# Kernel optimization log

Hardware: AMD Instinct MI355X
Metric: run time of the kernel (lower is better)

Reference implementation:

```python
import jax, jax.numpy as jnp
import numpy as np

EPS = 1e-12  # matches torch F.normalize eps

def _l2norm(v, axis):
    n = jnp.sqrt(jnp.sum(v * v, axis=axis, keepdims=True))
    return v / jnp.maximum(n, EPS)

def setup_inputs() -> dict:
    key = jax.random.key(0)
    k1, k2, k3 = jax.random.split(key, 3)
    N, D, H, W, K = 64, 128, 60, 80, 64
    x = jax.random.normal(k1, (N, D, H, W), dtype=jnp.float32)
    conv_w = jax.random.normal(k2, (K, D), dtype=jnp.float32) * 0.1
    centroids = jax.random.uniform(k3, (K, D), dtype=jnp.float32)
    return {"x": x, "conv_w": conv_w, "centroids": centroids}

def reference(x, conv_w, centroids):
    N, D, H, W = x.shape
    K = conv_w.shape[0]
    # descriptor-wise L2 normalization over channel dim
    x = _l2norm(x, axis=1)
    xf = x.reshape(N, D, H * W)                       # [N, D, P]
    # 1x1 conv (no bias) == matmul over channels, then softmax over clusters
    logits = jnp.einsum('kd,ndp->nkp', conv_w, xf)    # [N, K, P]
    sa = jax.nn.softmax(logits, axis=1)               # [N, K, P]
    # vlad[n,k,:] = sum_p sa[n,k,p] * (xf[n,:,p] - centroids[k])
    agg = jnp.einsum('nkp,ndp->nkd', sa, xf)          # [N, K, D]
    vlad = agg - sa.sum(axis=-1)[..., None] * centroids[None]
    vlad = _l2norm(vlad, axis=2)                      # intra-normalization
    vlad = vlad.reshape(N, K * D)
    vlad = _l2norm(vlad, axis=1)                      # global L2 norm
    return vlad
```

## Files before the change

kernel.cpp:

```cpp
#include <hip/hip_runtime.h>
#include <hip/hip_bf16.h>
#include <math.h>

#define NN 64
#define DD 128
#define PP 4800
#define KK 64
#define BPN 15
#define PB  320
#define CP  64
#define NCH 5

#define WT  136
#define XPT 136
#define XDT 72
#define SAT 72

#define PAGG_SZ  ((size_t)NN * BPN * KK * DD)
#define PSSUM_SZ ((size_t)NN * BPN * KK)
#define VTMP_SZ  ((size_t)NN * KK * DD)
#define GSUM_SZ  ((size_t)NN * 8)

typedef __attribute__((ext_vector_type(8))) short bf16x8;
typedef __attribute__((ext_vector_type(4))) float f32x4;

__device__ __forceinline__ unsigned short f2bf(float f) {
  unsigned u = __float_as_uint(f);
  u += 0x7fffu + ((u >> 16) & 1u);
  return (unsigned short)(u >> 16);
}
__device__ __forceinline__ unsigned pk2(float a, float b) {
  union { __hip_bfloat162 h2; unsigned u; } cv;
  cv.h2 = __float22bfloat162_rn(make_float2(a, b));
  return cv.u;
}

__global__ __launch_bounds__(256, 2) void main_kernel(const float* __restrict__ x,
                                                      const float* __restrict__ conv_w,
                                                      float* __restrict__ pagg,
                                                      float* __restrict__ pssum) {
  __shared__ __align__(16) unsigned short w_s[KK * WT];
  __shared__ __align__(16) unsigned short xpd[CP * XPT];
  __shared__ __align__(16) unsigned short xdp[DD * XDT];
  __shared__ __align__(16) unsigned short sa_s[KK * SAT];
  __shared__ float red_s[256];

  const int b = blockIdx.x;
  const int n = b / BPN, sl = b % BPN;
  const int t = threadIdx.x, lane = t & 63, wv = t >> 6;
  const int lq = lane >> 4, ll = lane & 15;
  const int pb = t & 7, db = t >> 3;

  {
    int k = t >> 2, h = t & 3;
    const float* wp = conv_w + k * DD + h * 32;
    unsigned short* dst = &w_s[k * WT + h * 32];
#pragma unroll
    for (int i = 0; i < 4; ++i) {
      float4 a = *(const float4*)(wp + 8 * i);
      float4 c = *(const float4*)(wp + 8 * i + 4);
      uint4 o = {pk2(a.x, a.y), pk2(a.z, a.w), pk2(c.x, c.y), pk2(c.z, c.w)};
      *(uint4*)&dst[8 * i] = o;
    }
  }
  if (t < 64) red_s[t] = 0.f;

  const float* xb = x + (size_t)n * DD * PP + (size_t)(4 * db) * PP + sl * PB + 8 * pb;

  float4 pf[8];
#pragma unroll
  for (int r = 0; r < 4; ++r) {
    pf[2 * r]     = *(const float4*)(xb + (size_t)r * PP);
    pf[2 * r + 1] = *(const float4*)(xb + (size_t)r * PP + 4);
  }

  f32x4 acc[8];
#pragma unroll
  for (int i = 0; i < 8; ++i) acc[i] = (f32x4){0.f, 0.f, 0.f, 0.f};
  float ssacc[16];
#pragma unroll
  for (int i = 0; i < 16; ++i) ssacc[i] = 0.f;

  for (int c = 0; c < NCH; ++c) {
    float4 cur[8];
#pragma unroll
    for (int i = 0; i < 8; ++i) cur[i] = pf[i];
    if (c + 1 < NCH) {
      const float* xc = xb + (c + 1) * CP;
#pragma unroll
      for (int r = 0; r < 4; ++r) {
        pf[2 * r]     = *(const float4*)(xc + (size_t)r * PP);
        pf[2 * r + 1] = *(const float4*)(xc + (size_t)r * PP + 4);
      }
    }

    float sq[8];
#pragma unroll
    for (int h = 0; h < 2; ++h)
#pragma unroll
      for (int j = 0; j < 4; ++j) {
        float s = 0.f;
#pragma unroll
        for (int r = 0; r < 4; ++r) {
          float v = (&cur[2 * r + h].x)[j];
          s = fmaf(v, v, s);
        }
        sq[4 * h + j] = s;
      }
#pragma unroll
    for (int i = 0; i < 8; ++i) {
      sq[i] += __shfl_xor(sq[i], 8);
      sq[i] += __shfl_xor(sq[i], 16);
      sq[i] += __shfl_xor(sq[i], 32);
    }

    __syncthreads();

    if (lane < 8) {
#pragma unroll
      for (int j = 0; j < 8; ++j) atomicAdd(&red_s[8 * lane + j], sq[j]);
    }

    {
      unsigned prow[4][4];
#pragma unroll
      for (int r = 0; r < 4; ++r) {
        const float4& a = cur[2 * r];
        const float4& c2 = cur[2 * r + 1];
        prow[r][0] = pk2(a.x, a.y);
        prow[r][1] = pk2(a.z, a.w);
        prow[r][2] = pk2(c2.x, c2.y);
        prow[r][3] = pk2(c2.z, c2.w);
        uint4 o = {prow[r][0], prow[r][1], prow[r][2], prow[r][3]};
        *(uint4*)&xdp[(4 * db + r) * XDT + 8 * pb] = o;
      }
      const int colh = (((db >> 1) ^ pb) << 3) + (db & 1) * 4;
#pragma unroll
      for (int j2 = 0; j2 < 4; ++j2) {
        unsigned lo01 = __builtin_amdgcn_perm(prow[1][j2], prow[0][j2], 0x05040100u);
        unsigned hi01 = __builtin_amdgcn_perm(prow[1][j2], prow[0][j2], 0x07060302u);
        unsigned lo23 = __builtin_amdgcn_perm(prow[3][j2], prow[2][j2], 0x05040100u);
        unsigned hi23 = __builtin_amdgcn_perm(prow[3][j2], prow[2][j2], 0x07060302u);
        int p_e = 8 * pb + 2 * j2;
        *(uint2*)&xpd[p_e * XPT + colh]       = make_uint2(lo01, lo23);
        *(uint2*)&xpd[(p_e + 1) * XPT + colh] = make_uint2(hi01, hi23);
      }
    }
    __syncthreads();

    {
      const int prow_ = wv * 16 + ll;
      const int swz = (2 * wv + (ll >> 3)) & 7;
      f32x4 lg[4];
#pragma unroll
      for (int kt = 0; kt < 4; ++kt) lg[kt] = (f32x4){0.f, 0.f, 0.f, 0.f};
#pragma unroll
      for (int ks = 0; ks < 4; ++ks) {
        bf16x8 bfrag = *(const bf16x8*)&xpd[prow_ * XPT + ((((ks << 2) | lq) ^ swz) << 3)];
#pragma unroll
        for (int kt = 0; kt < 4; ++kt) {
          bf16x8 afrag = *(const bf16x8*)&w_s[(kt * 16 + ll) * WT + ks * 32 + lq * 8];
          lg[kt] = __builtin_amdgcn_mfma_f32_16x16x32_bf16(afrag, bfrag, lg[kt], 0, 0, 0);
        }
      }
      float iv = 1.0f / fmaxf(sqrtf(red_s[prow_]), 1e-12f);
      float vals[16];
      float m = -1e30f;
#pragma unroll
      for (int kt = 0; kt < 4; ++kt)
#pragma unroll
        for (int r = 0; r < 4; ++r) {
          float v = lg[kt][r] * iv;
          vals[kt * 4 + r] = v;
          m = fmaxf(m, v);
        }
      m = fmaxf(m, __shfl_xor(m, 16));
      m = fmaxf(m, __shfl_xor(m, 32));
      float se = 0.f;
#pragma unroll
      for (int i = 0; i < 16; ++i) {
        float e = __expf(vals[i] - m);
        vals[i] = e;
        se += e;
      }
      se += __shfl_xor(se, 16);
      se += __shfl_xor(se, 32);
      float rinv = 1.0f / se;
      float r2 = rinv * iv;
#pragma unroll
      for (int kt = 0; kt < 4; ++kt)
#pragma unroll
        for (int r = 0; r < 4; ++r) {
          float e = vals[kt * 4 + r];
          ssacc[kt * 4 + r] += e * rinv;
          sa_s[(kt * 16 + lq * 4 + r) * SAT + prow_] = f2bf(e * r2);
        }
    }
    __syncthreads();
    if (c + 1 < NCH && t < 64) red_s[t] = 0.f;

#pragma unroll
    for (int ks = 0; ks < 2; ++ks) {
      bf16x8 afrag = *(const bf16x8*)&sa_s[(wv * 16 + ll) * SAT + ks * 32 + lq * 8];
#pragma unroll
      for (int dt = 0; dt < 8; ++dt) {
        bf16x8 bfrag = *(const bf16x8*)&xdp[(dt * 16 + ll) * XDT + ks * 32 + lq * 8];
        acc[dt] = __builtin_amdgcn_mfma_f32_16x16x32_bf16(afrag, bfrag, acc[dt], 0, 0, 0);
      }
    }
  }

  {
    float* base = pagg + (size_t)(n * BPN + sl) * (KK * DD);
#pragma unroll
    for (int dt = 0; dt < 8; ++dt)
#pragma unroll
      for (int r = 0; r < 4; ++r)
        base[(16 * wv + 4 * lq + r) * DD + dt * 16 + ll] = acc[dt][r];
  }
#pragma unroll
  for (int i = 0; i < 16; ++i) {
    float s = ssacc[i];
    s += __shfl_xor(s, 1);
    s += __shfl_xor(s, 2);
    s += __shfl_xor(s, 4);
    s += __shfl_xor(s, 8);
    if (ll == 0) red_s[wv * 64 + (i >> 2) * 16 + lq * 4 + (i & 3)] = s;
  }
  __syncthreads();
  if (t < 64)
    pssum[(n * BPN + sl) * KK + t] =
        red_s[t] + red_s[64 + t] + red_s[128 + t] + red_s[192 + t];
}

__global__ __launch_bounds__(256) void ep1_kernel(const float* __restrict__ pagg,
                                                  const float* __restrict__ pssum,
                                                  const float* __restrict__ cent,
                                                  float* __restrict__ vtmp,
                                                  float* __restrict__ gsum) {
  __shared__ float wsum[4];
  const int blk = blockIdx.x;
  const int n = blk >> 3, kg = blk & 7;
  const int t = threadIdx.x;
  const int kl = t >> 5, c32 = t & 31;
  const int k = kg * 8 + kl;
  const size_t off = (size_t)k * DD + c32 * 4;

  const float* base = pagg + (size_t)n * BPN * (KK * DD) + off;
  float4 a = {0.f, 0.f, 0.f, 0.f};
  for (int s = 0; s < BPN; ++s) {
    float4 v = *(const float4*)(base + (size_t)s * (KK * DD));
    a.x += v.x; a.y += v.y; a.z += v.z; a.w += v.w;
  }
  float sk = 0.f;
  for (int s = 0; s < BPN; ++s) sk += pssum[(n * BPN + s) * KK + k];

  float4 c4 = *(const float4*)(cent + off);
  float4 v;
  v.x = fmaf(-sk, c4.x, a.x);
  v.y = fmaf(-sk, c4.y, a.y);
  v.z = fmaf(-sk, c4.z, a.z);
  v.w = fmaf(-sk, c4.w, a.w);

  float pss = v.x * v.x + v.y * v.y + v.z * v.z + v.w * v.w;
  float ss = pss;
  ss += __shfl_xor(ss, 1);
  ss += __shfl_xor(ss, 2);
  ss += __shfl_xor(ss, 4);
  ss += __shfl_xor(ss, 8);
  ss += __shfl_xor(ss, 16);
  float rinv = 1.0f / fmaxf(sqrtf(ss), 1e-12f);
  v.x *= rinv; v.y *= rinv; v.z *= rinv; v.w *= rinv;
  *(float4*)(vtmp + (size_t)n * (KK * DD) + off) = v;

  float gp = pss * rinv * rinv;
#pragma unroll
  for (int o = 1; o < 64; o <<= 1) gp += __shfl_xor(gp, o);
  if ((t & 63) == 0) wsum[t >> 6] = gp;
  __syncthreads();
  if (t == 0) gsum[blk] = wsum[0] + wsum[1] + wsum[2] + wsum[3];
}

__global__ __launch_bounds__(256) void ep2_kernel(const float* __restrict__ vtmp,
                                                  const float* __restrict__ gsum,
                                                  float* __restrict__ out) {
  const int n = blockIdx.x, t = threadIdx.x;
  const float* gs = gsum + n * 8;
  float g = gs[0] + gs[1] + gs[2] + gs[3] + gs[4] + gs[5] + gs[6] + gs[7];
  float ginv = 1.0f / fmaxf(sqrtf(g), 1e-12f);
  const float4* vi = (const float4*)(vtmp + (size_t)n * (KK * DD));
  float4* vo = (float4*)(out + (size_t)n * (KK * DD));
#pragma unroll
  for (int it = 0; it < 8; ++it) {
    int idx = t + 256 * it;
    float4 f = vi[idx];
    f.x *= ginv; f.y *= ginv; f.z *= ginv; f.w *= ginv;
    vo[idx] = f;
  }
}

extern "C" void kernel_launch(void* const* d_in, const int* in_sizes, int n_in,
                              void* d_out, int out_size, void* d_ws, size_t ws_size,
                              hipStream_t stream) {
  const float* x      = (const float*)d_in[0];
  const float* conv_w = (const float*)d_in[1];
  const float* cent   = (const float*)d_in[2];
  float* out = (float*)d_out;
  float* ws  = (float*)d_ws;

  float* pagg  = ws;
  float* pssum = pagg + PAGG_SZ;
  float* vtmp  = pssum + PSSUM_SZ;
  float* gsum  = vtmp + VTMP_SZ;

  main_kernel<<<NN * BPN, 256, 0, stream>>>(x, conv_w, pagg, pssum);
  ep1_kernel<<<NN * 8, 256, 0, stream>>>(pagg, pssum, cent, vtmp, gsum);
  ep2_kernel<<<NN, 256, 0, stream>>>(vtmp, gsum, out);
}
```

Before: 246.9 us.

## Store partial aggregates in fp16 and fold global norm into one epilogue

The per-slice partial VLAD aggregates are now written and read as fp16, which halves the workspace traffic between the main kernel and the epilogue. The second epilogue kernel is removed. Every intra-normalized cluster row has unit norm, so the global L2 norm over 64 rows equals 8, and the epilogue now multiplies by a constant 0.125 instead of reducing. This drops a kernel launch and the vtmp round trip. The costs are fp16 rounding in the partial sums, and a different result if any cluster row is exactly zero.

Measured after the change: 241.2 us. 1.02x faster.

```diff
diff --git a/kernel.cpp b/kernel.cpp
--- a/kernel.cpp
+++ b/kernel.cpp
@@ -1,5 +1,6 @@
 #include <hip/hip_runtime.h>
 #include <hip/hip_bf16.h>
+#include <hip/hip_fp16.h>
 #include <math.h>
 
 #define NN 64
@@ -18,8 +19,6 @@
 
 #define PAGG_SZ  ((size_t)NN * BPN * KK * DD)
 #define PSSUM_SZ ((size_t)NN * BPN * KK)
-#define VTMP_SZ  ((size_t)NN * KK * DD)
-#define GSUM_SZ  ((size_t)NN * 8)
 
 typedef __attribute__((ext_vector_type(8))) short bf16x8;
 typedef __attribute__((ext_vector_type(4))) float f32x4;
@@ -37,7 +36,7 @@
 
 __global__ __launch_bounds__(256, 2) void main_kernel(const float* __restrict__ x,
                                                       const float* __restrict__ conv_w,
-                                                      float* __restrict__ pagg,
+                                                      __half* __restrict__ pagg,
                                                       float* __restrict__ pssum) {
   __shared__ __align__(16) unsigned short w_s[KK * WT];
   __shared__ __align__(16) unsigned short xpd[CP * XPT];
@@ -211,12 +210,12 @@
   }
 
   {
-    float* base = pagg + (size_t)(n * BPN + sl) * (KK * DD);
+    __half* base = pagg + (size_t)(n * BPN + sl) * (KK * DD);
 #pragma unroll
     for (int dt = 0; dt < 8; ++dt)
 #pragma unroll
       for (int r = 0; r < 4; ++r)
-        base[(16 * wv + 4 * lq + r) * DD + dt * 16 + ll] = acc[dt][r];
+        base[(16 * wv + 4 * lq + r) * DD + dt * 16 + ll] = __float2half(acc[dt][r]);
   }
 #pragma unroll
   for (int i = 0; i < 16; ++i) {
@@ -233,12 +232,10 @@
         red_s[t] + red_s[64 + t] + red_s[128 + t] + red_s[192 + t];
 }
 
-__global__ __launch_bounds__(256) void ep1_kernel(const float* __restrict__ pagg,
-                                                  const float* __restrict__ pssum,
-                                                  const float* __restrict__ cent,
-                                                  float* __restrict__ vtmp,
-                                                  float* __restrict__ gsum) {
-  __shared__ float wsum[4];
+__global__ __launch_bounds__(256) void ep_kernel(const __half* __restrict__ pagg,
+                                                 const float* __restrict__ pssum,
+                                                 const float* __restrict__ cent,
+                                                 float* __restrict__ out) {
   const int blk = blockIdx.x;
   const int n = blk >> 3, kg = blk & 7;
   const int t = threadIdx.x;
@@ -246,11 +243,15 @@
   const int k = kg * 8 + kl;
   const size_t off = (size_t)k * DD + c32 * 4;
 
-  const float* base = pagg + (size_t)n * BPN * (KK * DD) + off;
+  const __half* base = pagg + (size_t)n * BPN * (KK * DD) + off;
   float4 a = {0.f, 0.f, 0.f, 0.f};
   for (int s = 0; s < BPN; ++s) {
-    float4 v = *(const float4*)(base + (size_t)s * (KK * DD));
-    a.x += v.x; a.y += v.y; a.z += v.z; a.w += v.w;
+    uint2 u = *(const uint2*)(base + (size_t)s * (KK * DD));
+    __half2 h0 = *(const __half2*)&u.x;
+    __half2 h1 = *(const __half2*)&u.y;
+    float2 f0 = __half22float2(h0);
+    float2 f1 = __half22float2(h1);
+    a.x += f0.x; a.y += f0.y; a.z += f1.x; a.w += f1.y;
   }
   float sk = 0.f;
   for (int s = 0; s < BPN; ++s) sk += pssum[(n * BPN + s) * KK + k];
@@ -262,41 +263,15 @@
   v.z = fmaf(-sk, c4.z, a.z);
   v.w = fmaf(-sk, c4.w, a.w);
 
-  float pss = v.x * v.x + v.y * v.y + v.z * v.z + v.w * v.w;
-  float ss = pss;
+  float ss = v.x * v.x + v.y * v.y + v.z * v.z + v.w * v.w;
   ss += __shfl_xor(ss, 1);
   ss += __shfl_xor(ss, 2);
   ss += __shfl_xor(ss, 4);
   ss += __shfl_xor(ss, 8);
   ss += __shfl_xor(ss, 16);
-  float rinv = 1.0f / fmaxf(sqrtf(ss), 1e-12f);
-  v.x *= rinv; v.y *= rinv; v.z *= rinv; v.w *= rinv;
-  *(float4*)(vtmp + (size_t)n * (KK * DD) + off) = v;
-
-  float gp = pss * rinv * rinv;
-#pragma unroll
-  for (int o = 1; o < 64; o <<= 1) gp += __shfl_xor(gp, o);
-  if ((t & 63) == 0) wsum[t >> 6] = gp;
-  __syncthreads();
-  if (t == 0) gsum[blk] = wsum[0] + wsum[1] + wsum[2] + wsum[3];
-}
-
-__global__ __launch_bounds__(256) void ep2_kernel(const float* __restrict__ vtmp,
-                                                  const float* __restrict__ gsum,
-                                                  float* __restrict__ out) {
-  const int n = blockIdx.x, t = threadIdx.x;
-  const float* gs = gsum + n * 8;
-  float g = gs[0] + gs[1] + gs[2] + gs[3] + gs[4] + gs[5] + gs[6] + gs[7];
-  float ginv = 1.0f / fmaxf(sqrtf(g), 1e-12f);
-  const float4* vi = (const float4*)(vtmp + (size_t)n * (KK * DD));
-  float4* vo = (float4*)(out + (size_t)n * (KK * DD));
-#pragma unroll
-  for (int it = 0; it < 8; ++it) {
-    int idx = t + 256 * it;
-    float4 f = vi[idx];
-    f.x *= ginv; f.y *= ginv; f.z *= ginv; f.w *= ginv;
-    vo[idx] = f;
-  }
+  float scale = 0.125f / fmaxf(sqrtf(ss), 1e-12f);
+  v.x *= scale; v.y *= scale; v.z *= scale; v.w *= scale;
+  *(float4*)(out + (size_t)n * (KK * DD) + off) = v;
 }
 
 extern "C" void kernel_launch(void* const* d_in, const int* in_sizes, int n_in,
@@ -308,12 +283,9 @@
   float* out = (float*)d_out;
   float* ws  = (float*)d_ws;
 
-  float* pagg  = ws;
-  float* pssum = pagg + PAGG_SZ;
-  float* vtmp  = pssum + PSSUM_SZ;
-  float* gsum  = vtmp + VTMP_SZ;
+  __half* pagg = (__half*)ws;
+  float* pssum = ws + PAGG_SZ / 2;
 
   main_kernel<<<NN * BPN, 256, 0, stream>>>(x, conv_w, pagg, pssum);
-  ep1_kernel<<<NN * 8, 256, 0, stream>>>(pagg, pssum, cent, vtmp, gsum);
-  ep2_kernel<<<NN, 256, 0, stream>>>(vtmp, gsum, out);
-}
+  ep_kernel<<<NN * 8, 256, 0, stream>>>(pagg, pssum, cent, out);
+}
```
